# Kernel tuning notes

Hardware: AMD Instinct MI355X
Metric: run time of the kernel (lower is better)

The kernel has to match this reference:

```python
import jax, jax.numpy as jnp
import numpy as np

B, C, H, W = 8, 512, 32, 32
HEADS, GROUPS, EPS = 8, 32, 1e-5


def setup_inputs() -> dict:
    key = jax.random.key(0)
    ks = jax.random.split(key, 8)
    s = 1.0 / np.sqrt(C)
    return {
        "hidden_states": jax.random.normal(ks[0], (B, C, H, W), jnp.float32),
        "gn_w": jnp.ones((C,), jnp.float32),
        "gn_b": jnp.zeros((C,), jnp.float32),
        "Wq": jax.random.normal(ks[1], (C, C), jnp.float32) * s,
        "Wk": jax.random.normal(ks[2], (C, C), jnp.float32) * s,
        "Wv": jax.random.normal(ks[3], (C, C), jnp.float32) * s,
        "Wo": jax.random.normal(ks[4], (C, C), jnp.float32) * s,
        "bo": jnp.zeros((C,), jnp.float32),
    }


def reference(hidden_states, gn_w, gn_b, Wq, Wk, Wv, Wo, bo):
    b, c, h, w = hidden_states.shape
    S = h * w
    d = c // HEADS
    # [B,C,H,W] -> [B,S,C]
    x = hidden_states.reshape(b, c, S).transpose(0, 2, 1)

    # GroupNorm over channels (applied on [B,C,S] layout): normalize per (group, spatial)
    xt = x.transpose(0, 2, 1).reshape(b, GROUPS, c // GROUPS, S)
    mu = jnp.mean(xt, axis=(2, 3), keepdims=True)
    var = jnp.var(xt, axis=(2, 3), keepdims=True)
    normed = ((xt - mu) * jax.lax.rsqrt(var + EPS)).reshape(b, c, S)
    normed = (normed * gn_w[None, :, None] + gn_b[None, :, None]).transpose(0, 2, 1)  # [B,S,C]

    # Projections: query from normed states, key/value from raw encoder(=hidden) states
    q = (normed @ Wq.T).reshape(b, S, HEADS, d)
    k = (x @ Wk.T).reshape(b, S, HEADS, d)
    v = (x @ Wv.T).reshape(b, S, HEADS, d)

    scale = d ** -0.5
    scores = jnp.einsum("bshd,bthd->bhst", q, k) * scale  # [B,H,S,S]
    probs = jax.nn.softmax(scores.astype(jnp.float32), axis=-1)  # fp32 softmax (also stored)
    ctx = jnp.einsum("bhst,bthd->bshd", probs.astype(v.dtype), v).reshape(b, S, c)

    out = ctx @ Wo.T + bo  # to_out[0]; to_out[1] is dropout (identity at eval)
    return out.transpose(0, 2, 1).reshape(b, c, h, w)
```

## Files before the change

kernel.cpp:

```cpp
#include <hip/hip_runtime.h>
#include <hip/hip_bf16.h>

typedef short bf16x8 __attribute__((ext_vector_type(8)));
typedef short s16x4  __attribute__((ext_vector_type(4)));
typedef float f32x4  __attribute__((ext_vector_type(4)));

#define NB 8
#define NC 512
#define NS 1024
#define NH 8
#define DH 64
#define GN_GROUPS 32
#define GN_EPS 1e-5f

#if __has_builtin(__builtin_amdgcn_exp2f)
#define EXP2(x) __builtin_amdgcn_exp2f(x)
#else
#define EXP2(x) __expf((x) * 0.69314718056f)
#endif

static __device__ __forceinline__ short f2bf(float f) {
  union { __hip_bfloat16 h; short s; } u;
  u.h = __float2bfloat16(f);
  return u.s;
}

static __device__ __forceinline__ int pack2bf_fast(float a, float b) {
  unsigned ua = __float_as_uint(a) + 0x8000u;
  unsigned ub = __float_as_uint(b) + 0x8000u;
  return (int)__builtin_amdgcn_perm(ub, ua, 0x07060302u);
}

static __device__ __forceinline__ void async_lds16(const void* g, void* l) {
  __builtin_amdgcn_global_load_lds((__attribute__((address_space(1))) void*)(g),
                                   (__attribute__((address_space(3))) void*)(l),
                                   16, 0, 0);
}

#define MFMA16(a, b, c) __builtin_amdgcn_mfma_f32_16x16x32_bf16((a), (b), (c), 0, 0, 0)

__global__ void wconv4(const float4* __restrict__ Wq, const float4* __restrict__ Wk,
                       const float4* __restrict__ Wv, const float4* __restrict__ Wo,
                       s16x4* __restrict__ oq, s16x4* __restrict__ ok,
                       s16x4* __restrict__ ov, s16x4* __restrict__ oo, float qscale) {
  int sel = blockIdx.x >> 8;
  int i = (blockIdx.x & 255) * 256 + threadIdx.x;
  const float4* src = (sel == 0) ? Wq : (sel == 1) ? Wk : (sel == 2) ? Wv : Wo;
  s16x4* dst        = (sel == 0) ? oq : (sel == 1) ? ok : (sel == 2) ? ov : oo;
  float scale = (sel == 0) ? qscale : 1.0f;
  float4 f = src[i];
  s16x4 o;
  o[0] = f2bf(f.x * scale); o[1] = f2bf(f.y * scale);
  o[2] = f2bf(f.z * scale); o[3] = f2bf(f.w * scale);
  dst[i] = o;
}

__global__ __launch_bounds__(256) void gn_stats(const float* __restrict__ x,
                                                float* __restrict__ stats) {
  int bg = blockIdx.x;
  const float4* p = (const float4*)(x + (size_t)bg * 16384);
  float s = 0.f, s2 = 0.f;
  for (int i = threadIdx.x; i < 4096; i += 256) {
    float4 v = p[i];
    s  += v.x + v.y + v.z + v.w;
    s2 += v.x * v.x + v.y * v.y + v.z * v.z + v.w * v.w;
  }
  for (int off = 32; off > 0; off >>= 1) {
    s  += __shfl_down(s, off, 64);
    s2 += __shfl_down(s2, off, 64);
  }
  __shared__ float red[8];
  int w = threadIdx.x >> 6;
  if ((threadIdx.x & 63) == 0) { red[w * 2] = s; red[w * 2 + 1] = s2; }
  __syncthreads();
  if (threadIdx.x == 0) {
    float S = 0.f, S2 = 0.f;
    for (int i = 0; i < 4; i++) { S += red[i * 2]; S2 += red[i * 2 + 1]; }
    float mu  = S / 16384.f;
    float var = S2 / 16384.f - mu * mu;
    stats[bg * 2]     = mu;
    stats[bg * 2 + 1] = rsqrtf(var + GN_EPS);
  }
}

__global__ __launch_bounds__(256) void tnorm(const float* __restrict__ x,
                                             const float* __restrict__ stats,
                                             const float* __restrict__ gw,
                                             const float* __restrict__ gb,
                                             short* __restrict__ xT,
                                             short* __restrict__ nT) {
  __shared__ float tile[64 * 65];
  int b = blockIdx.z, c0 = blockIdx.y * 64, s0 = blockIdx.x * 64;
  int t = threadIdx.x;
  const float* xp = x + ((size_t)b * NC + c0) * NS + s0;
#pragma unroll
  for (int p = 0; p < 4; p++) {
    int idx = p * 256 + t;
    int cl = idx >> 4;
    int s4 = (idx & 15) * 4;
    float4 v = *(const float4*)(xp + (size_t)cl * NS + s4);
    tile[cl * 65 + s4 + 0] = v.x;
    tile[cl * 65 + s4 + 1] = v.y;
    tile[cl * 65 + s4 + 2] = v.z;
    tile[cl * 65 + s4 + 3] = v.w;
  }
  __syncthreads();
#pragma unroll
  for (int p = 0; p < 4; p++) {
    int idx = p * 256 + t;
    int sl = idx >> 4;
    int c4 = (idx & 15) * 4;
    size_t ob = ((size_t)b * NS + s0 + sl) * NC + c0 + c4;
    s16x4 xo, no;
#pragma unroll
    for (int j = 0; j < 4; j++) {
      int c = c0 + c4 + j;
      float val = tile[(c4 + j) * 65 + sl];
      int g = c >> 4;
      float mu = stats[(b * GN_GROUPS + g) * 2];
      float rs = stats[(b * GN_GROUPS + g) * 2 + 1];
      float nv = (val - mu) * rs * gw[c] + gb[c];
      xo[j] = f2bf(val);
      no[j] = f2bf(nv);
    }
    *(s16x4*)(xT + ob) = xo;
    *(s16x4*)(nT + ob) = no;
  }
}

__global__ __launch_bounds__(256) void gemm_qkv(const short* __restrict__ nT,
                                                const short* __restrict__ xT,
                                                const short* __restrict__ wq,
                                                const short* __restrict__ wk,
                                                const short* __restrict__ wv,
                                                short* __restrict__ q,
                                                short* __restrict__ k,
                                                short* __restrict__ v) {
  __shared__ __attribute__((aligned(16))) short sA[128 * 32];
  __shared__ __attribute__((aligned(16))) short sB[128 * 32];
  int proj = blockIdx.y >> 2;
  int n0 = (blockIdx.y & 3) * 128;
  int m0 = blockIdx.x * 128;
  const short* A  = (proj == 0) ? nT : xT;
  const short* Bm = (proj == 0) ? wq : ((proj == 1) ? wk : wv);
  short* Out      = (proj == 0) ? q  : ((proj == 1) ? k  : v);

  int tid = threadIdx.x, lane = tid & 63, w = tid >> 6;
  int quad = lane >> 4, l16 = lane & 15;
  int m_off = (w >> 1) * 64, n_off = (w & 1) * 64;
  int sr4 = lane >> 2;
  int csw = ((lane & 3) ^ ((sr4 >> 1) & 3)) * 8;
  int rsw = (quad ^ ((l16 >> 1) & 3)) * 8;

  const short* gA = A  + ((size_t)(m0 + w * 32 + sr4)) * 512 + csw;
  const short* gB = Bm + ((size_t)(n0 + w * 32 + sr4)) * 512 + csw;
  short* lA = &sA[w * 1024];
  short* lB = &sB[w * 1024];

  f32x4 acc[4][4] = {};

  for (int kk = 0; kk < 512; kk += 32) {
    __syncthreads();
    async_lds16(gA + kk,            lA);
    async_lds16(gA + kk + 16 * 512, lA + 512);
    async_lds16(gB + kk,            lB);
    async_lds16(gB + kk + 16 * 512, lB + 512);
    __syncthreads();
    bf16x8 aF[4], bF[4];
#pragma unroll
    for (int ms = 0; ms < 4; ms++)
      aF[ms] = *(const bf16x8*)&sA[(m_off + ms * 16 + l16) * 32 + rsw];
#pragma unroll
    for (int ns = 0; ns < 4; ns++)
      bF[ns] = *(const bf16x8*)&sB[(n_off + ns * 16 + l16) * 32 + rsw];
#pragma unroll
    for (int ms = 0; ms < 4; ms++)
#pragma unroll
      for (int ns = 0; ns < 4; ns++)
        acc[ms][ns] = MFMA16(aF[ms], bF[ns], acc[ms][ns]);
  }
#pragma unroll
  for (int ms = 0; ms < 4; ms++)
#pragma unroll
    for (int ns = 0; ns < 4; ns++)
#pragma unroll
      for (int r = 0; r < 4; r++) {
        int row = m0 + m_off + ms * 16 + quad * 4 + r;
        int col = n0 + n_off + ns * 16 + l16;
        Out[(size_t)row * 512 + col] = f2bf(acc[ms][ns][r]);
      }
}

__global__ __launch_bounds__(256) void vtrans(const short* __restrict__ v,
                                              short* __restrict__ vT) {
  __shared__ __attribute__((aligned(16))) short t[64 * 72];
  int b = blockIdx.y >> 3, h = blockIdx.y & 7;
  int s0 = blockIdx.x * 64;
  int tid = threadIdx.x;
  int row = tid >> 2, ch = (tid & 3) * 8;
  const short* vp = v + (size_t)(b * NS + s0 + row) * NC + h * DH;
  *(bf16x8*)&t[row * 72 + ch]      = *(const bf16x8*)(vp + ch);
  *(bf16x8*)&t[row * 72 + ch + 32] = *(const bf16x8*)(vp + ch + 32);
  __syncthreads();
  int d = tid >> 2;
  short* op = vT + (size_t)((b * NH + h) * DH + d) * NS + s0;
#pragma unroll
  for (int half = 0; half < 2; half++) {
    int sc = (tid & 3) * 8 + half * 32;
    bf16x8 o;
#pragma unroll
    for (int j = 0; j < 8; j++) o[j] = t[(sc + j) * 72 + d];
    *(bf16x8*)(op + sc) = o;
  }
}

__global__ __launch_bounds__(256) void attn(const short* __restrict__ q,
                                            const short* __restrict__ k,
                                            const short* __restrict__ vT,
                                            short* __restrict__ ctx) {
  __shared__ __attribute__((aligned(16))) short smem[16384];
#define SK(p, hf) (&smem[((p) * 2 + (hf)) * 2048])
#define SV(p, c)  (&smem[8192 + ((p) * 2 + (c)) * 2048])
  int b = blockIdx.x >> 3, h = blockIdx.x & 7;
  int q0 = blockIdx.y * 128;
  int tid = threadIdx.x, lane = tid & 63, w = tid >> 6;
  int quad = lane >> 4, l16 = lane & 15;

  const short* kb = k  + (size_t)b * (NS * NC) + h * DH;
  const short* vb = vT + (size_t)(b * NH + h) * (DH * NS);

  bf16x8 qf[2][2];
#pragma unroll
  for (int g = 0; g < 2; g++) {
    const short* qp = q + ((size_t)(b * NS + q0 + g * 64 + w * 16 + l16)) * NC + h * DH + quad * 8;
    qf[g][0] = *(const bf16x8*)qp;
    qf[g][1] = *(const bf16x8*)(qp + 32);
  }

  int sr4  = lane >> 2;
  int srow = w * 16 + sr4;
  int csw  = ((lane & 3) ^ ((sr4 >> 1) & 3)) * 8;
  int rsw  = (quad ^ ((l16 >> 1) & 3)) * 8;

#define STAGE(p, kv0) do {                                             \
    const short* kg_ = kb + (size_t)((kv0) + srow) * NC + csw;         \
    async_lds16(kg_,      SK(p, 0) + w * 512);                         \
    async_lds16(kg_ + 32, SK(p, 1) + w * 512);                         \
    const short* vg_ = vb + (size_t)srow * NS + (kv0) + csw;           \
    async_lds16(vg_,      SV(p, 0) + w * 512);                         \
    async_lds16(vg_ + 32, SV(p, 1) + w * 512);                         \
  } while (0)

  STAGE(0, 0);

  f32x4 o[2][4] = {};
  float lsum[2] = {0.f, 0.f};
  int src0 = (quad & 1) * 32 + l16;
  int src1 = src0 + 16;
  int selB = quad >> 1;

  for (int kt = 0; kt < 16; kt++) {
    int p = kt & 1;
    __syncthreads();
    if (kt < 15) STAGE(1 - p, (kt + 1) * 64);

    f32x4 sc[2][4];
#pragma unroll
    for (int mt = 0; mt < 4; mt++) {
      bf16x8 ak0 = *(const bf16x8*)(SK(p, 0) + (mt * 16 + l16) * 32 + rsw);
      bf16x8 ak1 = *(const bf16x8*)(SK(p, 1) + (mt * 16 + l16) * 32 + rsw);
#pragma unroll
      for (int g = 0; g < 2; g++) {
        f32x4 z = {0.f, 0.f, 0.f, 0.f};
        z = MFMA16(ak0, qf[g][0], z);
        z = MFMA16(ak1, qf[g][1], z);
        sc[g][mt] = z;
      }
    }
    int pk[2][4][2];
#pragma unroll
    for (int g = 0; g < 2; g++)
#pragma unroll
      for (int mt = 0; mt < 4; mt++)
#pragma unroll
        for (int hh = 0; hh < 2; hh++) {
          float e0 = EXP2(sc[g][mt][2 * hh]);
          float e1 = EXP2(sc[g][mt][2 * hh + 1]);
          lsum[g] += e0 + e1;
          pk[g][mt][hh] = pack2bf_fast(e0, e1);
        }
    bf16x8 pf[2][2];
#pragma unroll
    for (int g = 0; g < 2; g++)
#pragma unroll
      for (int c = 0; c < 2; c++) {
        union { int d[4]; bf16x8 v; } u;
#pragma unroll
        for (int dd = 0; dd < 4; dd++) {
          int s = (dd >> 1) ? src1 : src0;
          int A = __shfl(pk[g][2 * c][dd & 1], s, 64);
          int B = __shfl(pk[g][2 * c + 1][dd & 1], s, 64);
          u.d[dd] = selB ? B : A;
        }
        pf[g][c] = u.v;
      }
#pragma unroll
    for (int dt = 0; dt < 4; dt++) {
      bf16x8 av0 = *(const bf16x8*)(SV(p, 0) + (dt * 16 + l16) * 32 + rsw);
      bf16x8 av1 = *(const bf16x8*)(SV(p, 1) + (dt * 16 + l16) * 32 + rsw);
#pragma unroll
      for (int g = 0; g < 2; g++) {
        o[g][dt] = MFMA16(av0, pf[g][0], o[g][dt]);
        o[g][dt] = MFMA16(av1, pf[g][1], o[g][dt]);
      }
    }
  }
#pragma unroll
  for (int g = 0; g < 2; g++) {
    lsum[g] += __shfl_xor(lsum[g], 16, 64);
    lsum[g] += __shfl_xor(lsum[g], 32, 64);
  }
  __syncthreads();
  short* sT = &smem[0];
#pragma unroll
  for (int g = 0; g < 2; g++) {
    float inv = 1.f / lsum[g];
#pragma unroll
    for (int dt = 0; dt < 4; dt++)
#pragma unroll
      for (int r = 0; r < 4; r++)
        sT[(g * 64 + w * 16 + l16) * 72 + dt * 16 + quad * 4 + r] = f2bf(o[g][dt][r] * inv);
  }
  __syncthreads();
  for (int it = tid; it < 1024; it += 256) {
    int row = it >> 3, ch = (it & 7) * 8;
    *(bf16x8*)&ctx[((size_t)(b * NS + q0 + row)) * NC + h * DH + ch] =
        *(const bf16x8*)&sT[row * 72 + ch];
  }
#undef STAGE
#undef SK
#undef SV
}

__global__ __launch_bounds__(256) void gemm_out(const short* __restrict__ ctx,
                                                const short* __restrict__ wo,
                                                const float* __restrict__ bo,
                                                float* __restrict__ out) {
  __shared__ __attribute__((aligned(16))) short sA[128 * 32];
  __shared__ __attribute__((aligned(16))) short sB[128 * 32];
  int n0 = blockIdx.y * 128;
  int m0 = blockIdx.x * 128;
  int tid = threadIdx.x, lane = tid & 63, w = tid >> 6;
  int quad = lane >> 4, l16 = lane & 15;
  int m_off = (w >> 1) * 64, n_off = (w & 1) * 64;
  int sr4 = lane >> 2;
  int csw = ((lane & 3) ^ ((sr4 >> 1) & 3)) * 8;
  int rsw = (quad ^ ((l16 >> 1) & 3)) * 8;

  const short* gA = ctx + ((size_t)(m0 + w * 32 + sr4)) * 512 + csw;
  const short* gB = wo  + ((size_t)(n0 + w * 32 + sr4)) * 512 + csw;
  short* lA = &sA[w * 1024];
  short* lB = &sB[w * 1024];

  f32x4 acc[4][4] = {};

  for (int kk = 0; kk < 512; kk += 32) {
    __syncthreads();
    async_lds16(gA + kk,            lA);
    async_lds16(gA + kk + 16 * 512, lA + 512);
    async_lds16(gB + kk,            lB);
    async_lds16(gB + kk + 16 * 512, lB + 512);
    __syncthreads();
    bf16x8 aF[4], bF[4];
#pragma unroll
    for (int ms = 0; ms < 4; ms++)
      aF[ms] = *(const bf16x8*)&sA[(m_off + ms * 16 + l16) * 32 + rsw];
#pragma unroll
    for (int ns = 0; ns < 4; ns++)
      bF[ns] = *(const bf16x8*)&sB[(n_off + ns * 16 + l16) * 32 + rsw];
#pragma unroll
    for (int ms = 0; ms < 4; ms++)
#pragma unroll
      for (int ns = 0; ns < 4; ns++)
        acc[ms][ns] = MFMA16(aF[ms], bF[ns], acc[ms][ns]);
  }
#pragma unroll
  for (int ms = 0; ms < 4; ms++)
#pragma unroll
    for (int ns = 0; ns < 4; ns++)
#pragma unroll
      for (int r = 0; r < 4; r++) {
        int row = m0 + m_off + ms * 16 + quad * 4 + r;
        int col = n0 + n_off + ns * 16 + l16;
        int bb = row >> 10, s = row & 1023;
        out[((size_t)(bb * NC + col)) * NS + s] = acc[ms][ns][r] + bo[col];
      }
}

extern "C" void kernel_launch(void* const* d_in, const int* in_sizes, int n_in,
                              void* d_out, int out_size, void* d_ws, size_t ws_size,
                              hipStream_t stream) {
  const float* x  = (const float*)d_in[0];
  const float* gw = (const float*)d_in[1];
  const float* gb = (const float*)d_in[2];
  const float* Wq = (const float*)d_in[3];
  const float* Wk = (const float*)d_in[4];
  const float* Wv = (const float*)d_in[5];
  const float* Wo = (const float*)d_in[6];
  const float* bo = (const float*)d_in[7];
  float* out = (float*)d_out;

  char* ws = (char*)d_ws;
  const size_t MAT = (size_t)8192 * 512 * 2;
  float* stats = (float*)ws;
  short* xT  = (short*)(ws + 4096);
  short* nT  = (short*)(ws + 4096 + 1 * MAT);
  short* q   = (short*)(ws + 4096 + 2 * MAT);
  short* k   = (short*)(ws + 4096 + 3 * MAT);
  short* v   = (short*)(ws + 4096 + 4 * MAT);
  short* ctx = (short*)(ws + 4096 + 5 * MAT);
  short* wqb = (short*)(ws + 4096 + 6 * MAT);
  short* wkb = wqb + 262144;
  short* wvb = wkb + 262144;
  short* wob = wvb + 262144;
  short* vt  = nT;

  const float qscale = 0.125f * 1.44269504088896f;
  wconv4<<<1024, 256, 0, stream>>>((const float4*)Wq, (const float4*)Wk,
                                   (const float4*)Wv, (const float4*)Wo,
                                   (s16x4*)wqb, (s16x4*)wkb, (s16x4*)wvb, (s16x4*)wob,
                                   qscale);
  gn_stats<<<256, 256, 0, stream>>>(x, stats);
  tnorm<<<dim3(16, 8, 8), 256, 0, stream>>>(x, stats, gw, gb, xT, nT);
  gemm_qkv<<<dim3(64, 12), 256, 0, stream>>>(nT, xT, wqb, wkb, wvb, q, k, v);
  vtrans<<<dim3(16, 64), 256, 0, stream>>>(v, vt);
  attn<<<dim3(64, 8), 256, 0, stream>>>(q, k, vt, ctx);
  gemm_out<<<dim3(64, 4), 256, 0, stream>>>(ctx, wob, bo, out);
}
```

Measured before the change: 167.0 us.

## Split attention KV across two warp groups, fuse prep kernels, write V transposed

Merges the weight-conversion and GroupNorm-stats kernels into one launch. The QKV GEMM now writes V directly in the [B,H,D,S] layout, which drops the separate vtrans kernel. The attention kernel grows to 512 threads, with two 4-wave groups each covering half of the KV sequence; their partial outputs and row sums are combined through LDS at the end. The output GEMM uses 64-row tiles so it launches twice as many blocks. These changes aim to cut launch count and extra memory passes and to raise parallelism, at the cost of more LDS per attention block and an extra reduction step.

```diff
diff --git a/kernel.cpp b/kernel.cpp
--- a/kernel.cpp
+++ b/kernel.cpp
@@ -39,47 +39,52 @@
 
 #define MFMA16(a, b, c) __builtin_amdgcn_mfma_f32_16x16x32_bf16((a), (b), (c), 0, 0, 0)
 
-__global__ void wconv4(const float4* __restrict__ Wq, const float4* __restrict__ Wk,
-                       const float4* __restrict__ Wv, const float4* __restrict__ Wo,
-                       s16x4* __restrict__ oq, s16x4* __restrict__ ok,
-                       s16x4* __restrict__ ov, s16x4* __restrict__ oo, float qscale) {
-  int sel = blockIdx.x >> 8;
-  int i = (blockIdx.x & 255) * 256 + threadIdx.x;
-  const float4* src = (sel == 0) ? Wq : (sel == 1) ? Wk : (sel == 2) ? Wv : Wo;
-  s16x4* dst        = (sel == 0) ? oq : (sel == 1) ? ok : (sel == 2) ? ov : oo;
-  float scale = (sel == 0) ? qscale : 1.0f;
-  float4 f = src[i];
-  s16x4 o;
-  o[0] = f2bf(f.x * scale); o[1] = f2bf(f.y * scale);
-  o[2] = f2bf(f.z * scale); o[3] = f2bf(f.w * scale);
-  dst[i] = o;
-}
-
-__global__ __launch_bounds__(256) void gn_stats(const float* __restrict__ x,
-                                                float* __restrict__ stats) {
-  int bg = blockIdx.x;
-  const float4* p = (const float4*)(x + (size_t)bg * 16384);
-  float s = 0.f, s2 = 0.f;
-  for (int i = threadIdx.x; i < 4096; i += 256) {
-    float4 v = p[i];
-    s  += v.x + v.y + v.z + v.w;
-    s2 += v.x * v.x + v.y * v.y + v.z * v.z + v.w * v.w;
-  }
-  for (int off = 32; off > 0; off >>= 1) {
-    s  += __shfl_down(s, off, 64);
-    s2 += __shfl_down(s2, off, 64);
-  }
-  __shared__ float red[8];
-  int w = threadIdx.x >> 6;
-  if ((threadIdx.x & 63) == 0) { red[w * 2] = s; red[w * 2 + 1] = s2; }
-  __syncthreads();
-  if (threadIdx.x == 0) {
-    float S = 0.f, S2 = 0.f;
-    for (int i = 0; i < 4; i++) { S += red[i * 2]; S2 += red[i * 2 + 1]; }
-    float mu  = S / 16384.f;
-    float var = S2 / 16384.f - mu * mu;
-    stats[bg * 2]     = mu;
-    stats[bg * 2 + 1] = rsqrtf(var + GN_EPS);
+__global__ __launch_bounds__(256) void prep(const float* __restrict__ x,
+                                            float* __restrict__ stats,
+                                            const float4* __restrict__ Wq,
+                                            const float4* __restrict__ Wk,
+                                            const float4* __restrict__ Wv,
+                                            const float4* __restrict__ Wo,
+                                            s16x4* __restrict__ oq, s16x4* __restrict__ ok,
+                                            s16x4* __restrict__ ov, s16x4* __restrict__ oo,
+                                            float qscale) {
+  if (blockIdx.x < 256) {
+    int bg = blockIdx.x;
+    const float4* p = (const float4*)(x + (size_t)bg * 16384);
+    float s = 0.f, s2 = 0.f;
+    for (int i = threadIdx.x; i < 4096; i += 256) {
+      float4 v = p[i];
+      s  += v.x + v.y + v.z + v.w;
+      s2 += v.x * v.x + v.y * v.y + v.z * v.z + v.w * v.w;
+    }
+    for (int off = 32; off > 0; off >>= 1) {
+      s  += __shfl_down(s, off, 64);
+      s2 += __shfl_down(s2, off, 64);
+    }
+    __shared__ float red[8];
+    int w = threadIdx.x >> 6;
+    if ((threadIdx.x & 63) == 0) { red[w * 2] = s; red[w * 2 + 1] = s2; }
+    __syncthreads();
+    if (threadIdx.x == 0) {
+      float S = 0.f, S2 = 0.f;
+      for (int i = 0; i < 4; i++) { S += red[i * 2]; S2 += red[i * 2 + 1]; }
+      float mu  = S / 16384.f;
+      float var = S2 / 16384.f - mu * mu;
+      stats[bg * 2]     = mu;
+      stats[bg * 2 + 1] = rsqrtf(var + GN_EPS);
+    }
+  } else {
+    int idx = blockIdx.x - 256;
+    int sel = idx >> 8;
+    int i = (idx & 255) * 256 + threadIdx.x;
+    const float4* src = (sel == 0) ? Wq : (sel == 1) ? Wk : (sel == 2) ? Wv : Wo;
+    s16x4* dst        = (sel == 0) ? oq : (sel == 1) ? ok : (sel == 2) ? ov : oo;
+    float scale = (sel == 0) ? qscale : 1.0f;
+    float4 f = src[i];
+    s16x4 o;
+    o[0] = f2bf(f.x * scale); o[1] = f2bf(f.y * scale);
+    o[2] = f2bf(f.z * scale); o[3] = f2bf(f.w * scale);
+    dst[i] = o;
   }
 }
 
@@ -135,7 +140,7 @@
                                                 const short* __restrict__ wv,
                                                 short* __restrict__ q,
                                                 short* __restrict__ k,
-                                                short* __restrict__ v) {
+                                                short* __restrict__ vt) {
   __shared__ __attribute__((aligned(16))) short sA[128 * 32];
   __shared__ __attribute__((aligned(16))) short sB[128 * 32];
   int proj = blockIdx.y >> 2;
@@ -143,7 +148,7 @@
   int m0 = blockIdx.x * 128;
   const short* A  = (proj == 0) ? nT : xT;
   const short* Bm = (proj == 0) ? wq : ((proj == 1) ? wk : wv);
-  short* Out      = (proj == 0) ? q  : ((proj == 1) ? k  : v);
+  short* Out      = (proj == 0) ? q  : ((proj == 1) ? k  : vt);
 
   int tid = threadIdx.x, lane = tid & 63, w = tid >> 6;
   int quad = lane >> 4, l16 = lane & 15;
@@ -179,51 +184,44 @@
       for (int ns = 0; ns < 4; ns++)
         acc[ms][ns] = MFMA16(aF[ms], bF[ns], acc[ms][ns]);
   }
-#pragma unroll
-  for (int ms = 0; ms < 4; ms++)
-#pragma unroll
-    for (int ns = 0; ns < 4; ns++)
-#pragma unroll
-      for (int r = 0; r < 4; r++) {
-        int row = m0 + m_off + ms * 16 + quad * 4 + r;
-        int col = n0 + n_off + ns * 16 + l16;
-        Out[(size_t)row * 512 + col] = f2bf(acc[ms][ns][r]);
-      }
-}
-
-__global__ __launch_bounds__(256) void vtrans(const short* __restrict__ v,
-                                              short* __restrict__ vT) {
-  __shared__ __attribute__((aligned(16))) short t[64 * 72];
-  int b = blockIdx.y >> 3, h = blockIdx.y & 7;
-  int s0 = blockIdx.x * 64;
-  int tid = threadIdx.x;
-  int row = tid >> 2, ch = (tid & 3) * 8;
-  const short* vp = v + (size_t)(b * NS + s0 + row) * NC + h * DH;
-  *(bf16x8*)&t[row * 72 + ch]      = *(const bf16x8*)(vp + ch);
-  *(bf16x8*)&t[row * 72 + ch + 32] = *(const bf16x8*)(vp + ch + 32);
-  __syncthreads();
-  int d = tid >> 2;
-  short* op = vT + (size_t)((b * NH + h) * DH + d) * NS + s0;
-#pragma unroll
-  for (int half = 0; half < 2; half++) {
-    int sc = (tid & 3) * 8 + half * 32;
-    bf16x8 o;
-#pragma unroll
-    for (int j = 0; j < 8; j++) o[j] = t[(sc + j) * 72 + d];
-    *(bf16x8*)(op + sc) = o;
-  }
-}
-
-__global__ __launch_bounds__(256) void attn(const short* __restrict__ q,
-                                            const short* __restrict__ k,
-                                            const short* __restrict__ vT,
-                                            short* __restrict__ ctx) {
-  __shared__ __attribute__((aligned(16))) short smem[16384];
-#define SK(p, hf) (&smem[((p) * 2 + (hf)) * 2048])
-#define SV(p, c)  (&smem[8192 + ((p) * 2 + (c)) * 2048])
+  if (proj < 2) {
+#pragma unroll
+    for (int ms = 0; ms < 4; ms++)
+#pragma unroll
+      for (int ns = 0; ns < 4; ns++)
+#pragma unroll
+        for (int r = 0; r < 4; r++) {
+          int row = m0 + m_off + ms * 16 + quad * 4 + r;
+          int col = n0 + n_off + ns * 16 + l16;
+          Out[(size_t)row * 512 + col] = f2bf(acc[ms][ns][r]);
+        }
+  } else {
+#pragma unroll
+    for (int ms = 0; ms < 4; ms++)
+#pragma unroll
+      for (int ns = 0; ns < 4; ns++) {
+        int rowb = m0 + m_off + ms * 16 + quad * 4;
+        int col  = n0 + n_off + ns * 16 + l16;
+        int bb = rowb >> 10, s = rowb & 1023;
+        s16x4 pk4;
+#pragma unroll
+        for (int r = 0; r < 4; r++) pk4[r] = f2bf(acc[ms][ns][r]);
+        *(s16x4*)&Out[((size_t)(bb * NC + col)) * NS + s] = pk4;
+      }
+  }
+}
+
+__global__ __launch_bounds__(512, 4) void attn(const short* __restrict__ q,
+                                               const short* __restrict__ k,
+                                               const short* __restrict__ vT,
+                                               short* __restrict__ ctx) {
+  __shared__ __attribute__((aligned(16))) short smem[32768];
+#define SKp(wg, p, hf) (&smem[((wg) * 4 + (p) * 2 + (hf)) * 2048])
+#define SVp(wg, p, c)  (&smem[16384 + ((wg) * 4 + (p) * 2 + (c)) * 2048])
   int b = blockIdx.x >> 3, h = blockIdx.x & 7;
   int q0 = blockIdx.y * 128;
   int tid = threadIdx.x, lane = tid & 63, w = tid >> 6;
+  int wg = w >> 2, wl = w & 3;
   int quad = lane >> 4, l16 = lane & 15;
 
   const short* kb = k  + (size_t)b * (NS * NC) + h * DH;
@@ -232,23 +230,24 @@
   bf16x8 qf[2][2];
 #pragma unroll
   for (int g = 0; g < 2; g++) {
-    const short* qp = q + ((size_t)(b * NS + q0 + g * 64 + w * 16 + l16)) * NC + h * DH + quad * 8;
+    const short* qp = q + ((size_t)(b * NS + q0 + g * 64 + wl * 16 + l16)) * NC + h * DH + quad * 8;
     qf[g][0] = *(const bf16x8*)qp;
     qf[g][1] = *(const bf16x8*)(qp + 32);
   }
 
   int sr4  = lane >> 2;
-  int srow = w * 16 + sr4;
+  int srow = wl * 16 + sr4;
   int csw  = ((lane & 3) ^ ((sr4 >> 1) & 3)) * 8;
   int rsw  = (quad ^ ((l16 >> 1) & 3)) * 8;
 
-#define STAGE(p, kv0) do {                                             \
-    const short* kg_ = kb + (size_t)((kv0) + srow) * NC + csw;         \
-    async_lds16(kg_,      SK(p, 0) + w * 512);                         \
-    async_lds16(kg_ + 32, SK(p, 1) + w * 512);                         \
-    const short* vg_ = vb + (size_t)srow * NS + (kv0) + csw;           \
-    async_lds16(vg_,      SV(p, 0) + w * 512);                         \
-    async_lds16(vg_ + 32, SV(p, 1) + w * 512);                         \
+#define STAGE(p, kt) do {                                              \
+    int kv0_ = (wg * 8 + (kt)) * 64;                                   \
+    const short* kg_ = kb + (size_t)(kv0_ + srow) * NC + csw;          \
+    async_lds16(kg_,      SKp(wg, p, 0) + wl * 512);                   \
+    async_lds16(kg_ + 32, SKp(wg, p, 1) + wl * 512);                   \
+    const short* vg_ = vb + (size_t)srow * NS + kv0_ + csw;            \
+    async_lds16(vg_,      SVp(wg, p, 0) + wl * 512);                   \
+    async_lds16(vg_ + 32, SVp(wg, p, 1) + wl * 512);                   \
   } while (0)
 
   STAGE(0, 0);
@@ -259,16 +258,16 @@
   int src1 = src0 + 16;
   int selB = quad >> 1;
 
-  for (int kt = 0; kt < 16; kt++) {
+  for (int kt = 0; kt < 8; kt++) {
     int p = kt & 1;
     __syncthreads();
-    if (kt < 15) STAGE(1 - p, (kt + 1) * 64);
+    if (kt < 7) STAGE(1 - p, kt + 1);
 
     f32x4 sc[2][4];
 #pragma unroll
     for (int mt = 0; mt < 4; mt++) {
-      bf16x8 ak0 = *(const bf16x8*)(SK(p, 0) + (mt * 16 + l16) * 32 + rsw);
-      bf16x8 ak1 = *(const bf16x8*)(SK(p, 1) + (mt * 16 + l16) * 32 + rsw);
+      bf16x8 ak0 = *(const bf16x8*)(SKp(wg, p, 0) + (mt * 16 + l16) * 32 + rsw);
+      bf16x8 ak1 = *(const bf16x8*)(SKp(wg, p, 1) + (mt * 16 + l16) * 32 + rsw);
 #pragma unroll
       for (int g = 0; g < 2; g++) {
         f32x4 z = {0.f, 0.f, 0.f, 0.f};
@@ -306,8 +305,8 @@
       }
 #pragma unroll
     for (int dt = 0; dt < 4; dt++) {
-      bf16x8 av0 = *(const bf16x8*)(SV(p, 0) + (dt * 16 + l16) * 32 + rsw);
-      bf16x8 av1 = *(const bf16x8*)(SV(p, 1) + (dt * 16 + l16) * 32 + rsw);
+      bf16x8 av0 = *(const bf16x8*)(SVp(wg, p, 0) + (dt * 16 + l16) * 32 + rsw);
+      bf16x8 av1 = *(const bf16x8*)(SVp(wg, p, 1) + (dt * 16 + l16) * 32 + rsw);
 #pragma unroll
       for (int g = 0; g < 2; g++) {
         o[g][dt] = MFMA16(av0, pf[g][0], o[g][dt]);
@@ -320,78 +319,101 @@
     lsum[g] += __shfl_xor(lsum[g], 16, 64);
     lsum[g] += __shfl_xor(lsum[g], 32, 64);
   }
+  float* dump  = (float*)smem;
+  float* lsums = (float*)&smem[16384];
+  __syncthreads();
+  if (wg == 1) {
+#pragma unroll
+    for (int g = 0; g < 2; g++) {
+#pragma unroll
+      for (int dt = 0; dt < 4; dt++)
+        *(f32x4*)&dump[((((g * 4 + wl) * 4) + dt) * 64 + lane) * 4] = o[g][dt];
+      if (quad == 0) lsums[(g * 4 + wl) * 16 + l16] = lsum[g];
+    }
+  }
+  __syncthreads();
+  float inv[2];
+  if (wg == 0) {
+#pragma unroll
+    for (int g = 0; g < 2; g++) {
+      inv[g] = 1.f / (lsum[g] + lsums[(g * 4 + wl) * 16 + l16]);
+#pragma unroll
+      for (int dt = 0; dt < 4; dt++) {
+        f32x4 add = *(const f32x4*)&dump[((((g * 4 + wl) * 4) + dt) * 64 + lane) * 4];
+        o[g][dt] += add;
+      }
+    }
+  }
   __syncthreads();
   short* sT = &smem[0];
-#pragma unroll
-  for (int g = 0; g < 2; g++) {
-    float inv = 1.f / lsum[g];
-#pragma unroll
-    for (int dt = 0; dt < 4; dt++)
-#pragma unroll
-      for (int r = 0; r < 4; r++)
-        sT[(g * 64 + w * 16 + l16) * 72 + dt * 16 + quad * 4 + r] = f2bf(o[g][dt][r] * inv);
+  if (wg == 0) {
+#pragma unroll
+    for (int g = 0; g < 2; g++)
+#pragma unroll
+      for (int dt = 0; dt < 4; dt++)
+#pragma unroll
+        for (int r = 0; r < 4; r++)
+          sT[(g * 64 + wl * 16 + l16) * 72 + dt * 16 + quad * 4 + r] = f2bf(o[g][dt][r] * inv[g]);
   }
   __syncthreads();
-  for (int it = tid; it < 1024; it += 256) {
+  for (int it = tid; it < 1024; it += 512) {
     int row = it >> 3, ch = (it & 7) * 8;
     *(bf16x8*)&ctx[((size_t)(b * NS + q0 + row)) * NC + h * DH + ch] =
         *(const bf16x8*)&sT[row * 72 + ch];
   }
 #undef STAGE
-#undef SK
-#undef SV
+#undef SKp
+#undef SVp
 }
 
 __global__ __launch_bounds__(256) void gemm_out(const short* __restrict__ ctx,
                                                 const short* __restrict__ wo,
                                                 const float* __restrict__ bo,
                                                 float* __restrict__ out) {
-  __shared__ __attribute__((aligned(16))) short sA[128 * 32];
+  __shared__ __attribute__((aligned(16))) short sA[64 * 32];
   __shared__ __attribute__((aligned(16))) short sB[128 * 32];
   int n0 = blockIdx.y * 128;
-  int m0 = blockIdx.x * 128;
+  int m0 = blockIdx.x * 64;
   int tid = threadIdx.x, lane = tid & 63, w = tid >> 6;
   int quad = lane >> 4, l16 = lane & 15;
-  int m_off = (w >> 1) * 64, n_off = (w & 1) * 64;
   int sr4 = lane >> 2;
   int csw = ((lane & 3) ^ ((sr4 >> 1) & 3)) * 8;
   int rsw = (quad ^ ((l16 >> 1) & 3)) * 8;
 
-  const short* gA = ctx + ((size_t)(m0 + w * 32 + sr4)) * 512 + csw;
+  const short* gA = ctx + ((size_t)(m0 + w * 16 + sr4)) * 512 + csw;
   const short* gB = wo  + ((size_t)(n0 + w * 32 + sr4)) * 512 + csw;
-  short* lA = &sA[w * 1024];
+  short* lA = &sA[w * 512];
   short* lB = &sB[w * 1024];
 
-  f32x4 acc[4][4] = {};
+  f32x4 acc[4][2] = {};
 
   for (int kk = 0; kk < 512; kk += 32) {
     __syncthreads();
     async_lds16(gA + kk,            lA);
-    async_lds16(gA + kk + 16 * 512, lA + 512);
     async_lds16(gB + kk,            lB);
     async_lds16(gB + kk + 16 * 512, lB + 512);
     __syncthreads();
-    bf16x8 aF[4], bF[4];
-#pragma unroll
-    for (int ms = 0; ms < 4; ms++)
-      aF[ms] = *(const bf16x8*)&sA[(m_off + ms * 16 + l16) * 32 + rsw];
-#pragma unroll
-    for (int ns = 0; ns < 4; ns++)
-      bF[ns] = *(const bf16x8*)&sB[(n_off + ns * 16 + l16) * 32 + rsw];
-#pragma unroll
-    for (int ms = 0; ms < 4; ms++)
-#pragma unroll
-      for (int ns = 0; ns < 4; ns++)
+    bf16x8 aF[4], bF[2];
+#pragma unroll
+    for (int ms = 0; ms < 4; ms++)
+      aF[ms] = *(const bf16x8*)&sA[(ms * 16 + l16) * 32 + rsw];
+#pragma unroll
+    for (int ns = 0; ns < 2; ns++)
+      bF[ns] = *(const bf16x8*)&sB[(w * 32 + ns * 16 + l16) * 32 + rsw];
+#pragma unroll
+    for (int ms = 0; ms < 4; ms++)
+#pragma unroll
+      for (int ns = 0; ns < 2; ns++)
         acc[ms][ns] = MFMA16(aF[ms], bF[ns], acc[ms][ns]);
   }
 #pragma unroll
   for (int ms = 0; ms < 4; ms++)
 #pragma unroll
-    for (int ns = 0; ns < 4; ns++)
+    for (int ns = 0; ns < 2; ns++)
 #pragma unroll
       for (int r = 0; r < 4; r++) {
-        int row = m0 + m_off + ms * 16 + quad * 4 + r;
-        int col = n0 + n_off + ns * 16 + l16;
+        int row = m0 + ms * 16 + quad * 4 + r;
+        int col = n0 + w * 32 + ns * 16 + l16;
         int bb = row >> 10, s = row & 1023;
         out[((size_t)(bb * NC + col)) * NS + s] = acc[ms][ns][r] + bo[col];
       }
@@ -417,23 +439,21 @@
   short* nT  = (short*)(ws + 4096 + 1 * MAT);
   short* q   = (short*)(ws + 4096 + 2 * MAT);
   short* k   = (short*)(ws + 4096 + 3 * MAT);
-  short* v   = (short*)(ws + 4096 + 4 * MAT);
+  short* vt  = (short*)(ws + 4096 + 4 * MAT);
   short* ctx = (short*)(ws + 4096 + 5 * MAT);
   short* wqb = (short*)(ws + 4096 + 6 * MAT);
   short* wkb = wqb + 262144;
   short* wvb = wkb + 262144;
   short* wob = wvb + 262144;
-  short* vt  = nT;
 
   const float qscale = 0.125f * 1.44269504088896f;
-  wconv4<<<1024, 256, 0, stream>>>((const float4*)Wq, (const float4*)Wk,
-                                   (const float4*)Wv, (const float4*)Wo,
-                                   (s16x4*)wqb, (s16x4*)wkb, (s16x4*)wvb, (s16x4*)wob,
-                                   qscale);
-  gn_stats<<<256, 256, 0, stream>>>(x, stats);
+  prep<<<1280, 256, 0, stream>>>(x, stats,
+                                 (const float4*)Wq, (const float4*)Wk,
+                                 (const float4*)Wv, (const float4*)Wo,
+                                 (s16x4*)wqb, (s16x4*)wkb, (s16x4*)wvb, (s16x4*)wob,
+                                 qscale);
   tnorm<<<dim3(16, 8, 8), 256, 0, stream>>>(x, stats, gw, gb, xT, nT);
-  gemm_qkv<<<dim3(64, 12), 256, 0, stream>>>(nT, xT, wqb, wkb, wvb, q, k, v);
-  vtrans<<<dim3(16, 64), 256, 0, stream>>>(v, vt);
-  attn<<<dim3(64, 8), 256, 0, stream>>>(q, k, vt, ctx);
-  gemm_out<<<dim3(64, 4), 256, 0, stream>>>(ctx, wob, bo, out);
-}
+  gemm_qkv<<<dim3(64, 12), 256, 0, stream>>>(nT, xT, wqb, wkb, wvb, q, k, vt);
+  attn<<<dim3(64, 8), 512, 0, stream>>>(q, k, vt, ctx);
+  gemm_out<<<dim3(128, 4), 256, 0, stream>>>(ctx, wob, bo, out);
+}
```

New measurement: 150.2 us. -10.1%, faster.
